# Optimization experiments

Measured on AMD Instinct MI355X. Metric: run time of the kernel, lower is better.

## Reference

```python
import jax, jax.numpy as jnp
import numpy as np


def setup_inputs() -> dict:
    key = jax.random.key(0)
    k1, k2, k3, k4, k5 = jax.random.split(key, 5)
    NNZ = 1_600_000
    N, IN, OUT = 8192, 4096, 4096
    vals = jax.random.normal(k1, (NNZ,), dtype=jnp.float32)
    rows = jax.random.randint(k2, (NNZ,), 0, N, dtype=jnp.int32)
    cols = jax.random.randint(k3, (NNZ,), 0, IN, dtype=jnp.int32)
    # kaiming_uniform-ish init scale for weight, uniform bias
    bound_w = jnp.sqrt(1.0 / IN)
    weight = jax.random.uniform(k4, (OUT, IN), dtype=jnp.float32, minval=-bound_w, maxval=bound_w)
    bias = jax.random.uniform(k5, (OUT,), dtype=jnp.float32, minval=-bound_w, maxval=bound_w)
    return {"vals": vals, "rows": rows, "cols": cols, "weight": weight, "bias": bias, "n_rows": N}


def reference(vals, rows, cols, weight, bias, n_rows):
    """Sparse COO [n_rows, in_features] @ weight.T + bias (torch.sparse.addmm).

    Densify via scatter-add (COO semantics: duplicate indices accumulate),
    then a single dense GEMM which dominates the cost.
    """
    in_features = weight.shape[1]
    dense = jnp.zeros((n_rows, in_features), dtype=vals.dtype).at[rows, cols].add(vals)
    return dense @ weight.T + bias  # [n_rows, out_features]
```

## Files before the change

### kernel.cpp

```cpp
#include <hip/hip_runtime.h>

typedef __attribute__((ext_vector_type(8)))  __bf16 bf16x8;
typedef __attribute__((ext_vector_type(16))) float  f32x16;
typedef __attribute__((ext_vector_type(4)))  float  f32x4;
typedef __attribute__((ext_vector_type(8)))  unsigned short u16x8;

__device__ inline unsigned short f2bf(float f) {
    unsigned int u = __float_as_uint(f);
    u += 0x7FFFu + ((u >> 16) & 1u);
    return (unsigned short)(u >> 16);
}

__global__ __launch_bounds__(256) void scatter_cvt(
        const float* __restrict__ vals,
        const int* __restrict__ rows,
        const int* __restrict__ cols,
        unsigned short* __restrict__ Ab,
        int nnz, int in_f,
        const float* __restrict__ wsrc,
        unsigned short* __restrict__ wdst,
        long nW, int cvtBlocks) {
    if ((int)blockIdx.x < cvtBlocks) {
        long i = ((long)blockIdx.x * 256 + threadIdx.x) * 8;
        if (i + 8 <= nW) {
            f32x4 a = *(const f32x4*)(wsrc + i);
            f32x4 b = *(const f32x4*)(wsrc + i + 4);
            u16x8 o;
            o[0] = f2bf(a[0]); o[1] = f2bf(a[1]); o[2] = f2bf(a[2]); o[3] = f2bf(a[3]);
            o[4] = f2bf(b[0]); o[5] = f2bf(b[1]); o[6] = f2bf(b[2]); o[7] = f2bf(b[3]);
            *(u16x8*)(wdst + i) = o;
        }
        return;
    }
    int i = ((int)blockIdx.x - cvtBlocks) * 256 + threadIdx.x;
    if (i >= nnz) return;
    float v = vals[i];
    size_t idx = (size_t)rows[i] * in_f + cols[i];
#if __has_builtin(__builtin_amdgcn_global_atomic_fadd_v2bf16)
    typedef __attribute__((ext_vector_type(2))) short s16x2;
    unsigned short hv = f2bf(v);
    s16x2 add;
    add[0] = (idx & 1) ? (short)0 : (short)hv;
    add[1] = (idx & 1) ? (short)hv : (short)0;
    __builtin_amdgcn_global_atomic_fadd_v2bf16(
        (__attribute__((address_space(1))) s16x2*)(Ab + (idx & ~(size_t)1)), add);
#else
    unsigned int* word = (unsigned int*)(Ab + (idx & ~(size_t)1));
    unsigned int sh = (unsigned int)(idx & 1) * 16u;
    unsigned int old = *word, assumed;
    do {
        assumed = old;
        unsigned int cur = (assumed >> sh) & 0xFFFFu;
        float f = __uint_as_float(cur << 16) + v;
        unsigned int nb = f2bf(f);
        unsigned int repl = (assumed & ~(0xFFFFu << sh)) | (nb << sh);
        old = atomicCAS(word, assumed, repl);
    } while (old != assumed);
#endif
}


__device__ __forceinline__ bf16x8 read_frag(const unsigned short* hb, int rowl, int slot) {
    int cs = slot ^ (rowl & 7);
    return *(const bf16x8*)(hb + rowl * 64 + (cs << 3));
}

__device__ __forceinline__ void stage_half(const unsigned short* __restrict__ G,
                                           int grow0, int K, int kbase,
                                           unsigned short* hb, int tid) {
    const int lane = tid & 63, wv = tid >> 6;
    #pragma unroll
    for (int j = 0; j < 2; ++j) {
        int u = j * 512 + wv * 64 + lane;
        int rowl = u >> 3;
        int c = (u & 7) ^ (rowl & 7);
        const unsigned short* g = G + (size_t)(grow0 + rowl) * K + kbase + c * 8;
        unsigned short* l = hb + (size_t)(j * 512 + wv * 64) * 8;
        __builtin_amdgcn_global_load_lds(
            (const __attribute__((address_space(1))) void*)g,
            (__attribute__((address_space(3))) void*)l, 16, 0, 0);
    }
}

__global__ __launch_bounds__(512, 2) void gemm_bt_bias(
    const unsigned short* __restrict__ A,
    const unsigned short* __restrict__ B,
    const float* __restrict__ bias,
    float* __restrict__ C,
    int M, int N, int K)
{
    __shared__ unsigned short sA[2][2][8192];
    __shared__ unsigned short sB[2][2][8192];

    const int tid  = threadIdx.x;
    const int lane = tid & 63;
    const int wave = tid >> 6;
    const int wm = (wave >> 2) * 128;
    const int wn = (wave & 3) * 64;
    const int m32 = lane & 31;
    const int h   = lane >> 5;
    const int ah  = wm >> 7;
    const int bh  = wn >> 7;
    const int bro = wn & 64;

    const int nbx = gridDim.x;
    const int nwg = gridDim.x * gridDim.y;
    int flat = blockIdx.y * gridDim.x + blockIdx.x;
    int rid = (nwg & 7) ? flat : ((flat & 7) * (nwg >> 3) + (flat >> 3));
    const int bm = (rid / nbx) * 256;
    const int bn = (rid % nbx) * 256;

    f32x16 acc[4][2];
    #pragma unroll
    for (int i = 0; i < 4; ++i)
        #pragma unroll
        for (int j = 0; j < 2; ++j)
            #pragma unroll
            for (int r = 0; r < 16; ++r) acc[i][j][r] = 0.f;

    stage_half(A, bm,       K, 0,  &sA[0][0][0], tid);
    stage_half(A, bm + 128, K, 0,  &sA[0][1][0], tid);
    stage_half(B, bn,       K, 0,  &sB[0][0][0], tid);
    stage_half(B, bn + 128, K, 0,  &sB[0][1][0], tid);
    stage_half(A, bm,       K, 64, &sA[1][0][0], tid);
    stage_half(A, bm + 128, K, 64, &sA[1][1][0], tid);
    stage_half(B, bn,       K, 64, &sB[1][0][0], tid);
    stage_half(B, bn + 128, K, 64, &sB[1][1][0], tid);
    asm volatile("s_waitcnt vmcnt(8)" ::: "memory");
    __builtin_amdgcn_s_barrier();

    const int nt = K >> 6;
    for (int t = 0; t < nt; ++t) {
        const int cur = t & 1;
        const int t2k = ((t + 2 < nt) ? t + 2 : 0) << 6;
        const unsigned short* sAh = &sA[cur][ah][0];
        const unsigned short* sBh = &sB[cur][bh][0];

        {
            bf16x8 a0[4], a1[4], b0[2], b1[2];
            #pragma unroll
            for (int i = 0; i < 4; ++i) {
                int rl = i * 32 + m32;
                a0[i] = read_frag(sAh, rl, h);
                a1[i] = read_frag(sAh, rl, 2 + h);
            }
            #pragma unroll
            for (int j = 0; j < 2; ++j) {
                int rl = bro + j * 32 + m32;
                b0[j] = read_frag(sBh, rl, h);
                b1[j] = read_frag(sBh, rl, 2 + h);
            }
            __builtin_amdgcn_s_setprio(1);
            #pragma unroll
            for (int i = 0; i < 4; ++i)
                #pragma unroll
                for (int j = 0; j < 2; ++j)
                    acc[i][j] = __builtin_amdgcn_mfma_f32_32x32x16_bf16(a0[i], b0[j], acc[i][j], 0, 0, 0);
            #pragma unroll
            for (int i = 0; i < 4; ++i)
                #pragma unroll
                for (int j = 0; j < 2; ++j)
                    acc[i][j] = __builtin_amdgcn_mfma_f32_32x32x16_bf16(a1[i], b1[j], acc[i][j], 0, 0, 0);
            __builtin_amdgcn_s_setprio(0);
        }

        {
            bf16x8 a0[4], a1[4], b0[2], b1[2];
            #pragma unroll
            for (int i = 0; i < 4; ++i) {
                int rl = i * 32 + m32;
                a0[i] = read_frag(sAh, rl, 4 + h);
                a1[i] = read_frag(sAh, rl, 6 + h);
            }
            #pragma unroll
            for (int j = 0; j < 2; ++j) {
                int rl = bro + j * 32 + m32;
                b0[j] = read_frag(sBh, rl, 4 + h);
                b1[j] = read_frag(sBh, rl, 6 + h);
            }
            asm volatile("s_waitcnt vmcnt(0) lgkmcnt(0)" ::: "memory");
            __builtin_amdgcn_sched_barrier(0);
            __builtin_amdgcn_s_barrier();
            stage_half(A, bm,       K, t2k, &sA[cur][0][0], tid);
            stage_half(A, bm + 128, K, t2k, &sA[cur][1][0], tid);
            stage_half(B, bn,       K, t2k, &sB[cur][0][0], tid);
            stage_half(B, bn + 128, K, t2k, &sB[cur][1][0], tid);
            __builtin_amdgcn_s_setprio(1);
            #pragma unroll
            for (int i = 0; i < 4; ++i)
                #pragma unroll
                for (int j = 0; j < 2; ++j)
                    acc[i][j] = __builtin_amdgcn_mfma_f32_32x32x16_bf16(a0[i], b0[j], acc[i][j], 0, 0, 0);
            #pragma unroll
            for (int i = 0; i < 4; ++i)
                #pragma unroll
                for (int j = 0; j < 2; ++j)
                    acc[i][j] = __builtin_amdgcn_mfma_f32_32x32x16_bf16(a1[i], b1[j], acc[i][j], 0, 0, 0);
            __builtin_amdgcn_s_setprio(0);
        }
    }
    asm volatile("s_waitcnt vmcnt(0)" ::: "memory");

    #pragma unroll
    for (int j = 0; j < 2; ++j) {
        int col = bn + wn + j * 32 + m32;
        float bv = bias[col];
        #pragma unroll
        for (int i = 0; i < 4; ++i) {
            int rbase = bm + wm + i * 32 + 4 * h;
            #pragma unroll
            for (int r = 0; r < 16; ++r) {
                int row = rbase + (r & 3) + 8 * (r >> 2);
                __builtin_nontemporal_store(acc[i][j][r] + bv,
                                            &C[(size_t)row * N + col]);
            }
        }
    }
}

extern "C" void kernel_launch(void* const* d_in, const int* in_sizes, int n_in,
                              void* d_out, int out_size, void* d_ws, size_t ws_size,
                              hipStream_t stream) {
    const float* vals   = (const float*)d_in[0];
    const int*   rows   = (const int*)d_in[1];
    const int*   cols   = (const int*)d_in[2];
    const float* weight = (const float*)d_in[3];
    const float* bias   = (const float*)d_in[4];

    const int NNZ = in_sizes[0];
    const int OUT = in_sizes[4];
    const int IN  = in_sizes[3] / OUT;
    const int M   = out_size / OUT;

    unsigned short* Ab = (unsigned short*)d_ws;
    size_t abBytes = (size_t)M * IN * sizeof(unsigned short);
    unsigned short* Wb = (unsigned short*)((char*)d_ws + abBytes);

    hipMemsetAsync(Ab, 0, abBytes, stream);

    {
        long nW = (long)OUT * IN;
        int cvtBlocks = (int)((nW / 8 + 255) / 256);
        int scBlocks  = (NNZ + 255) / 256;
        scatter_cvt<<<cvtBlocks + scBlocks, 256, 0, stream>>>(
            vals, rows, cols, Ab, NNZ, IN, weight, Wb, nW, cvtBlocks);
    }

    dim3 grid(OUT / 256, M / 256);
    gemm_bt_bias<<<grid, 512, 0, stream>>>(Ab, Wb, bias, (float*)d_out, M, OUT, IN);
}
```

Baseline: 487.5 us.

## Software-pipeline LDS fragment reads across iterations with register double-buffering

Restructures the GEMM main loop so the fragments for the next half-tile are read from shared memory while the MFMAs for the current half run. Two register fragment sets alternate (X and Y), and the next tile's first half is prefetched right after the barrier. The goal is to hide LDS read latency behind matrix-core work. It costs extra vector registers, which may lower occupancy or cause spills, and it relies on the waitcnt placement staying correct when the next buffer is read after the barrier.

```diff
diff --git a/kernel.cpp b/kernel.cpp
--- a/kernel.cpp
+++ b/kernel.cpp
@@ -129,75 +129,93 @@
     asm volatile("s_waitcnt vmcnt(8)" ::: "memory");
     __builtin_amdgcn_s_barrier();
 
+    bf16x8 Xa0[4], Xa1[4], Xb0[2], Xb1[2];
+    bf16x8 Ya0[4], Ya1[4], Yb0[2], Yb1[2];
+
+    {
+        const unsigned short* sAh = &sA[0][ah][0];
+        const unsigned short* sBh = &sB[0][bh][0];
+        #pragma unroll
+        for (int i = 0; i < 4; ++i) {
+            int rl = i * 32 + m32;
+            Xa0[i] = read_frag(sAh, rl, h);
+            Xa1[i] = read_frag(sAh, rl, 2 + h);
+        }
+        #pragma unroll
+        for (int j = 0; j < 2; ++j) {
+            int rl = bro + j * 32 + m32;
+            Xb0[j] = read_frag(sBh, rl, h);
+            Xb1[j] = read_frag(sBh, rl, 2 + h);
+        }
+    }
+
     const int nt = K >> 6;
     for (int t = 0; t < nt; ++t) {
-        const int cur = t & 1;
+        const int cur = t & 1, nxt = cur ^ 1;
         const int t2k = ((t + 2 < nt) ? t + 2 : 0) << 6;
-        const unsigned short* sAh = &sA[cur][ah][0];
-        const unsigned short* sBh = &sB[cur][bh][0];
-
-        {
-            bf16x8 a0[4], a1[4], b0[2], b1[2];
-            #pragma unroll
-            for (int i = 0; i < 4; ++i) {
-                int rl = i * 32 + m32;
-                a0[i] = read_frag(sAh, rl, h);
-                a1[i] = read_frag(sAh, rl, 2 + h);
-            }
-            #pragma unroll
-            for (int j = 0; j < 2; ++j) {
-                int rl = bro + j * 32 + m32;
-                b0[j] = read_frag(sBh, rl, h);
-                b1[j] = read_frag(sBh, rl, 2 + h);
-            }
-            __builtin_amdgcn_s_setprio(1);
-            #pragma unroll
-            for (int i = 0; i < 4; ++i)
-                #pragma unroll
-                for (int j = 0; j < 2; ++j)
-                    acc[i][j] = __builtin_amdgcn_mfma_f32_32x32x16_bf16(a0[i], b0[j], acc[i][j], 0, 0, 0);
-            #pragma unroll
-            for (int i = 0; i < 4; ++i)
-                #pragma unroll
-                for (int j = 0; j < 2; ++j)
-                    acc[i][j] = __builtin_amdgcn_mfma_f32_32x32x16_bf16(a1[i], b1[j], acc[i][j], 0, 0, 0);
-            __builtin_amdgcn_s_setprio(0);
-        }
-
-        {
-            bf16x8 a0[4], a1[4], b0[2], b1[2];
-            #pragma unroll
-            for (int i = 0; i < 4; ++i) {
-                int rl = i * 32 + m32;
-                a0[i] = read_frag(sAh, rl, 4 + h);
-                a1[i] = read_frag(sAh, rl, 6 + h);
-            }
-            #pragma unroll
-            for (int j = 0; j < 2; ++j) {
-                int rl = bro + j * 32 + m32;
-                b0[j] = read_frag(sBh, rl, 4 + h);
-                b1[j] = read_frag(sBh, rl, 6 + h);
-            }
-            asm volatile("s_waitcnt vmcnt(0) lgkmcnt(0)" ::: "memory");
-            __builtin_amdgcn_sched_barrier(0);
-            __builtin_amdgcn_s_barrier();
-            stage_half(A, bm,       K, t2k, &sA[cur][0][0], tid);
-            stage_half(A, bm + 128, K, t2k, &sA[cur][1][0], tid);
-            stage_half(B, bn,       K, t2k, &sB[cur][0][0], tid);
-            stage_half(B, bn + 128, K, t2k, &sB[cur][1][0], tid);
-            __builtin_amdgcn_s_setprio(1);
-            #pragma unroll
-            for (int i = 0; i < 4; ++i)
-                #pragma unroll
-                for (int j = 0; j < 2; ++j)
-                    acc[i][j] = __builtin_amdgcn_mfma_f32_32x32x16_bf16(a0[i], b0[j], acc[i][j], 0, 0, 0);
-            #pragma unroll
-            for (int i = 0; i < 4; ++i)
-                #pragma unroll
-                for (int j = 0; j < 2; ++j)
-                    acc[i][j] = __builtin_amdgcn_mfma_f32_32x32x16_bf16(a1[i], b1[j], acc[i][j], 0, 0, 0);
-            __builtin_amdgcn_s_setprio(0);
-        }
+        const unsigned short* sAc = &sA[cur][ah][0];
+        const unsigned short* sBc = &sB[cur][bh][0];
+        const unsigned short* sAn = &sA[nxt][ah][0];
+        const unsigned short* sBn = &sB[nxt][bh][0];
+
+        #pragma unroll
+        for (int i = 0; i < 4; ++i) {
+            int rl = i * 32 + m32;
+            Ya0[i] = read_frag(sAc, rl, 4 + h);
+            Ya1[i] = read_frag(sAc, rl, 6 + h);
+        }
+        #pragma unroll
+        for (int j = 0; j < 2; ++j) {
+            int rl = bro + j * 32 + m32;
+            Yb0[j] = read_frag(sBc, rl, 4 + h);
+            Yb1[j] = read_frag(sBc, rl, 6 + h);
+        }
+        __builtin_amdgcn_sched_barrier(0);
+        __builtin_amdgcn_s_setprio(1);
+        #pragma unroll
+        for (int i = 0; i < 4; ++i)
+            #pragma unroll
+            for (int j = 0; j < 2; ++j)
+                acc[i][j] = __builtin_amdgcn_mfma_f32_32x32x16_bf16(Xa0[i], Xb0[j], acc[i][j], 0, 0, 0);
+        #pragma unroll
+        for (int i = 0; i < 4; ++i)
+            #pragma unroll
+            for (int j = 0; j < 2; ++j)
+                acc[i][j] = __builtin_amdgcn_mfma_f32_32x32x16_bf16(Xa1[i], Xb1[j], acc[i][j], 0, 0, 0);
+        __builtin_amdgcn_s_setprio(0);
+
+        asm volatile("s_waitcnt vmcnt(0) lgkmcnt(0)" ::: "memory");
+        __builtin_amdgcn_sched_barrier(0);
+        __builtin_amdgcn_s_barrier();
+        #pragma unroll
+        for (int i = 0; i < 4; ++i) {
+            int rl = i * 32 + m32;
+            Xa0[i] = read_frag(sAn, rl, h);
+            Xa1[i] = read_frag(sAn, rl, 2 + h);
+        }
+        #pragma unroll
+        for (int j = 0; j < 2; ++j) {
+            int rl = bro + j * 32 + m32;
+            Xb0[j] = read_frag(sBn, rl, h);
+            Xb1[j] = read_frag(sBn, rl, 2 + h);
+        }
+        stage_half(A, bm,       K, t2k, &sA[cur][0][0], tid);
+        stage_half(A, bm + 128, K, t2k, &sA[cur][1][0], tid);
+        stage_half(B, bn,       K, t2k, &sB[cur][0][0], tid);
+        stage_half(B, bn + 128, K, t2k, &sB[cur][1][0], tid);
+        __builtin_amdgcn_sched_barrier(0);
+        __builtin_amdgcn_s_setprio(1);
+        #pragma unroll
+        for (int i = 0; i < 4; ++i)
+            #pragma unroll
+            for (int j = 0; j < 2; ++j)
+                acc[i][j] = __builtin_amdgcn_mfma_f32_32x32x16_bf16(Ya0[i], Yb0[j], acc[i][j], 0, 0, 0);
+        #pragma unroll
+        for (int i = 0; i < 4; ++i)
+            #pragma unroll
+            for (int j = 0; j < 2; ++j)
+                acc[i][j] = __builtin_amdgcn_mfma_f32_32x32x16_bf16(Ya1[i], Yb1[j], acc[i][j], 0, 0, 0);
+        __builtin_amdgcn_s_setprio(0);
     }
     asm volatile("s_waitcnt vmcnt(0)" ::: "memory");
 
```

Measured after the change: 551.9 us. 1.13x slower.
